# Performance work log

Measured on AMD Instinct MI355X. Metric: run time of the kernel, lower is better.

The kernel has to match this reference:

```python
import jax, jax.numpy as jnp
import numpy as np

N_NODES = 100000
N_EDGES = 1600000
IN_DIM = 64
HIDDEN_DIM = 64


def setup_inputs() -> dict:
    key = jax.random.key(0)
    ks = jax.random.split(key, 8)
    x = jax.random.normal(ks[0], (N_NODES, IN_DIM), dtype=jnp.float32)
    edge_index = jax.random.randint(ks[1], (2, N_EDGES), 0, N_NODES, dtype=jnp.int32)
    s = 1.0 / np.sqrt(IN_DIM)
    sh = 1.0 / np.sqrt(HIDDEN_DIM)
    # SAGEConv params: lin_l (applied to mean-aggregated neighbors, with bias),
    # lin_r (applied to root/self features, no bias) -- PyG defaults.
    w1l = jax.random.uniform(ks[2], (IN_DIM, HIDDEN_DIM), jnp.float32, -s, s)
    b1l = jax.random.uniform(ks[3], (HIDDEN_DIM,), jnp.float32, -s, s)
    w1r = jax.random.uniform(ks[4], (IN_DIM, HIDDEN_DIM), jnp.float32, -s, s)
    w2l = jax.random.uniform(ks[5], (HIDDEN_DIM, HIDDEN_DIM), jnp.float32, -sh, sh)
    b2l = jax.random.uniform(ks[6], (HIDDEN_DIM,), jnp.float32, -sh, sh)
    w2r = jax.random.uniform(ks[7], (HIDDEN_DIM, HIDDEN_DIM), jnp.float32, -sh, sh)
    return {"x": x, "edge_index": edge_index, "w1l": w1l, "b1l": b1l,
            "w1r": w1r, "w2l": w2l, "b2l": b2l, "w2r": w2r}


def reference(x, edge_index, w1l, b1l, w1r, w2l, b2l, w2r):
    n = x.shape[0]
    src, dst = edge_index[0], edge_index[1]
    # in-degree (number of incoming messages per target node), clamped to 1
    deg = jax.ops.segment_sum(jnp.ones(src.shape, x.dtype), dst, num_segments=n)
    inv_deg = 1.0 / jnp.maximum(deg, 1.0)  # [N]

    def sage_conv(h, wl, bl, wr):
        # mean aggregation of neighbor messages: scatter-add then normalize
        agg = jax.ops.segment_sum(h[src], dst, num_segments=n) * inv_deg[:, None]
        return agg @ wl + bl + h @ wr

    h = jax.nn.relu(sage_conv(x, w1l, b1l, w1r))  # conv1 + relu
    return sage_conv(h, w2l, b2l, w2r)            # conv2 (no activation)
```

## Files before the change

kernel.cpp:

```cpp
#include <hip/hip_runtime.h>
#include <hip/hip_fp16.h>


#define DIM 64
#define BN 64
#define MAXBUCK 2048
#define CHUNK 8192
#define GCAP 2048
#define WT_STRIDE 72

using f16x8 = __attribute__((ext_vector_type(8))) _Float16;
using f32x4 = __attribute__((ext_vector_type(4))) float;

__device__ inline void addh8(float* acc, float4 raw) {
    const __half2* hp = (const __half2*)&raw;
#pragma unroll
    for (int k = 0; k < 4; ++k) {
        float2 f = __half22float2(hp[k]);
        acc[2 * k]     += f.x;
        acc[2 * k + 1] += f.y;
    }
}

__global__ __launch_bounds__(256) void prehist_kernel(const int* __restrict__ dst,
                                                      int* __restrict__ ghist,
                                                      int nE, int nbuck) {
    __shared__ int hist[MAXBUCK];
    const int t = threadIdx.x;
    for (int k = t; k < nbuck; k += 256) hist[k] = 0;
    __syncthreads();
    const int base = blockIdx.x * CHUNK;
    const int end = min(nE, base + CHUNK);
    for (int i = base + t; i < end; i += 256)
        atomicAdd(&hist[dst[i] >> 6], 1);
    __syncthreads();
    for (int k = t; k < nbuck; k += 256)
        if (hist[k]) atomicAdd(&ghist[k], hist[k]);
}

__global__ __launch_bounds__(1024) void scan_kernel(const int* __restrict__ ghist,
                                                    int* __restrict__ boff,
                                                    int* __restrict__ gcur, int nbuck) {
    __shared__ int sa[2048], sb[2048];
    const int t = threadIdx.x;
    int v0 = (t < nbuck) ? ghist[t] : 0;
    int v1 = (t + 1024 < nbuck) ? ghist[t + 1024] : 0;
    sa[t] = v0; sa[t + 1024] = v1;
    __syncthreads();
    int* in = sa; int* out = sb;
    for (int d = 1; d < 2048; d <<= 1) {
        out[t] = in[t] + ((t >= d) ? in[t - d] : 0);
        int i2 = t + 1024;
        out[i2] = in[i2] + ((i2 >= d) ? in[i2 - d] : 0);
        __syncthreads();
        int* tmp = in; in = out; out = tmp;
    }
    if (t < nbuck) { int e = in[t] - v0; boff[t] = e; gcur[t] = e; }
    if (t + 1024 < nbuck) { int e = in[t + 1024] - v1; boff[t + 1024] = e; gcur[t + 1024] = e; }
    if (t == 0) boff[nbuck] = in[2047];
}

__device__ inline void load_bfrag(const __half* __restrict__ H, long long nn, int lq,
                                  f16x8& b0, f16x8& b1) {
    b0 = *(const f16x8*)&H[nn * 64 + lq * 8];
    b1 = *(const f16x8*)&H[nn * 64 + 32 + lq * 8];
}
__device__ inline void load_bfrag(const float* __restrict__ H, long long nn, int lq,
                                  f16x8& b0, f16x8& b1) {
    const float* p = &H[nn * 64 + lq * 8];
    float4 u0 = *(const float4*)p;
    float4 u1 = *(const float4*)(p + 4);
    float4 u2 = *(const float4*)(p + 32);
    float4 u3 = *(const float4*)(p + 36);
    b0[0] = (_Float16)u0.x; b0[1] = (_Float16)u0.y; b0[2] = (_Float16)u0.z; b0[3] = (_Float16)u0.w;
    b0[4] = (_Float16)u1.x; b0[5] = (_Float16)u1.y; b0[6] = (_Float16)u1.z; b0[7] = (_Float16)u1.w;
    b1[0] = (_Float16)u2.x; b1[1] = (_Float16)u2.y; b1[2] = (_Float16)u2.z; b1[3] = (_Float16)u2.w;
    b1[4] = (_Float16)u3.x; b1[5] = (_Float16)u3.y; b1[6] = (_Float16)u3.z; b1[7] = (_Float16)u3.w;
}

template <typename InT>
__device__ void gemm_body(int bid, __half* wt,
                          const InT* __restrict__ H,
                          const float* __restrict__ Wl, const float* __restrict__ Wr,
                          const float* __restrict__ bias,
                          __half* __restrict__ A, __half* __restrict__ Dbuf, int n) {
    const int t = threadIdx.x;
    for (int i = t; i < 4096; i += 256) {
        int k = i >> 6, m = i & 63;
        wt[(size_t)m * WT_STRIDE + k] = __float2half(Wl[i]);
        wt[(size_t)(64 + m) * WT_STRIDE + k] = __float2half(Wr[i]);
    }
    __syncthreads();
    const int lane = t & 63, wave = t >> 6;
    const int ln = lane & 15, lq = lane >> 4;
    f16x8 af[2][4][2];
#pragma unroll
    for (int mat = 0; mat < 2; ++mat)
#pragma unroll
        for (int mt = 0; mt < 4; ++mt)
#pragma unroll
            for (int ki = 0; ki < 2; ++ki)
                af[mat][mt][ki] = *(const f16x8*)&wt[(size_t)(mat * 64 + mt * 16 + ln) * WT_STRIDE
                                                     + ki * 32 + lq * 8];
    float4 bf[4];
#pragma unroll
    for (int mt = 0; mt < 4; ++mt)
        bf[mt] = *(const float4*)&bias[mt * 16 + lq * 4];

    const int base = bid * 256;
    for (int it = 0; it < 4; ++it) {
        const int node = base + it * 64 + wave * 16 + ln;
        const long long nn = (node < n) ? node : (n - 1);
        f16x8 b0, b1;
        load_bfrag(H, nn, lq, b0, b1);
        f32x4 acc[2][4];
#pragma unroll
        for (int mat = 0; mat < 2; ++mat)
#pragma unroll
            for (int mt = 0; mt < 4; ++mt) {
                f32x4 z = {0.f, 0.f, 0.f, 0.f};
                z = __builtin_amdgcn_mfma_f32_16x16x32_f16(af[mat][mt][0], b0, z, 0, 0, 0);
                z = __builtin_amdgcn_mfma_f32_16x16x32_f16(af[mat][mt][1], b1, z, 0, 0, 0);
                acc[mat][mt] = z;
            }
        if (node < n) {
#pragma unroll
            for (int mt = 0; mt < 4; ++mt) {
                union { __half2 h[2]; float2 f; } u;
                u.h[0] = __floats2half2_rn(acc[0][mt][0], acc[0][mt][1]);
                u.h[1] = __floats2half2_rn(acc[0][mt][2], acc[0][mt][3]);
                *(float2*)&A[(size_t)node * 64 + mt * 16 + lq * 4] = u.f;
                union { __half2 h[2]; float2 f; } v;
                v.h[0] = __floats2half2_rn(acc[1][mt][0] + bf[mt].x, acc[1][mt][1] + bf[mt].y);
                v.h[1] = __floats2half2_rn(acc[1][mt][2] + bf[mt].z, acc[1][mt][3] + bf[mt].w);
                *(float2*)&Dbuf[(size_t)node * 64 + mt * 16 + lq * 4] = v.f;
            }
        }
    }
}

__global__ __launch_bounds__(256) void part_gemm_kernel(const int* __restrict__ src,
                                                        const int* __restrict__ dst,
                                                        int* __restrict__ gcur,
                                                        unsigned* __restrict__ P,
                                                        int nE, int nbuck, int pb,
                                                        const float* __restrict__ H,
                                                        const float* __restrict__ Wl,
                                                        const float* __restrict__ Wr,
                                                        const float* __restrict__ bias,
                                                        __half* __restrict__ A,
                                                        __half* __restrict__ Dbuf, int n) {
    __shared__ __align__(16) unsigned short smem_u[2 * 64 * WT_STRIDE];
    if ((int)blockIdx.x < pb) {
        int* hist = (int*)smem_u;
        const int t = threadIdx.x;
        for (int k = t; k < nbuck; k += 256) hist[k] = 0;
        __syncthreads();
        const int base = blockIdx.x * CHUNK;
        const int end = min(nE, base + CHUNK);
        for (int i = base + t; i < end; i += 256)
            atomicAdd(&hist[dst[i] >> 6], 1);
        __syncthreads();
        for (int k = t; k < nbuck; k += 256) {
            int h = hist[k];
            hist[k] = h ? atomicAdd(&gcur[k], h) : 0;
        }
        __syncthreads();
        for (int i = base + t; i < end; i += 256) {
            int d = dst[i];
            int bk = d >> 6;
            int pos = atomicAdd(&hist[bk], 1);
            P[pos] = ((unsigned)src[i] << 6) | (unsigned)(d & 63);
        }
    } else {
        gemm_body(blockIdx.x - pb, (__half*)smem_u, H, Wl, Wr, bias, A, Dbuf, n);
    }
}

__global__ __launch_bounds__(256) void gemm_kernel(const __half* __restrict__ H,
                                                   const float* __restrict__ Wl,
                                                   const float* __restrict__ Wr,
                                                   const float* __restrict__ bias,
                                                   __half* __restrict__ A,
                                                   __half* __restrict__ Dbuf, int n) {
    __shared__ __align__(16) unsigned short smem_u[2 * 64 * WT_STRIDE];
    gemm_body(blockIdx.x, (__half*)smem_u, H, Wl, Wr, bias, A, Dbuf, n);
}

template <bool RELU, typename OutT>
__global__ __launch_bounds__(256) void gather_sort_combine(const __half* __restrict__ A,
                                                           const __half* __restrict__ Dbuf,
                                                           const int* __restrict__ boff,
                                                           const unsigned* __restrict__ P,
                                                           int* __restrict__ spill,
                                                           OutT* __restrict__ out, int n) {
    __shared__ int hist[BN];
    __shared__ int rstart[BN];
    __shared__ int cur[BN];
    __shared__ int lsrc[GCAP];
    const int t = threadIdx.x;
    const int b = blockIdx.x;
    if (t < BN) hist[t] = 0;
    __syncthreads();
    const int start = boff[b], end = boff[b + 1];
    const int m = end - start;
    for (int i = start + t; i < end; i += 256)
        atomicAdd(&hist[P[i] & 63], 1);
    __syncthreads();
    if (t < 64) {
        int v = hist[t];
        int s = v;
#pragma unroll
        for (int d = 1; d < 64; d <<= 1) {
            int u = __shfl_up(s, d);
            if (t >= d) s += u;
        }
        rstart[t] = s - v;
        cur[t] = s - v;
    }
    __syncthreads();
    int* list = (m <= GCAP) ? (int*)lsrc : (spill + start);
    for (int i = start + t; i < end; i += 256) {
        unsigned p = P[i];
        int pos = atomicAdd(&cur[p & 63], 1);
        list[pos] = (int)(p >> 6);
    }
    __syncthreads();
    const int dg = t & 7;
    const size_t doff = (size_t)dg * 8;
    for (int pass = 0; pass < 2; ++pass) {
        const int r = pass * 32 + (t >> 3);
        const int node = b * BN + r;
        if (node >= n) continue;
        const int c = hist[r];
        const int* sp = list + rstart[r];
        float acc[8] = {0.f, 0.f, 0.f, 0.f, 0.f, 0.f, 0.f, 0.f};
        int j = 0;
        for (; j + 4 <= c; j += 4) {
            int e0 = sp[j + 0], e1 = sp[j + 1], e2 = sp[j + 2], e3 = sp[j + 3];
            float4 r0 = *(const float4*)&A[(size_t)e0 * 64 + doff];
            float4 r1 = *(const float4*)&A[(size_t)e1 * 64 + doff];
            float4 r2 = *(const float4*)&A[(size_t)e2 * 64 + doff];
            float4 r3 = *(const float4*)&A[(size_t)e3 * 64 + doff];
            addh8(acc, r0); addh8(acc, r1); addh8(acc, r2); addh8(acc, r3);
        }
        for (; j < c; ++j) {
            float4 rr = *(const float4*)&A[(size_t)sp[j] * 64 + doff];
            addh8(acc, rr);
        }
        const float inv = 1.0f / fmaxf((float)c, 1.0f);
        float d8[8] = {0, 0, 0, 0, 0, 0, 0, 0};
        addh8(d8, *(const float4*)&Dbuf[(size_t)node * 64 + doff]);
        float o[8];
#pragma unroll
        for (int k = 0; k < 8; ++k) {
            float v = fmaf(acc[k], inv, d8[k]);
            o[k] = RELU ? fmaxf(v, 0.f) : v;
        }
        if constexpr (sizeof(OutT) == 2) {
            union { __half2 h[4]; float4 f; } u;
#pragma unroll
            for (int k = 0; k < 4; ++k)
                u.h[k] = __floats2half2_rn(o[2 * k], o[2 * k + 1]);
            *(float4*)&out[(size_t)node * 64 + doff] = u.f;
        } else {
            *(float4*)&out[(size_t)node * 64 + doff]     = make_float4(o[0], o[1], o[2], o[3]);
            *(float4*)&out[(size_t)node * 64 + doff + 4] = make_float4(o[4], o[5], o[6], o[7]);
        }
    }
}

extern "C" void kernel_launch(void* const* d_in, const int* in_sizes, int n_in,
                              void* d_out, int out_size, void* d_ws, size_t ws_size,
                              hipStream_t stream) {
    const float* x   = (const float*)d_in[0];
    const int*   ei  = (const int*)d_in[1];
    const float* w1l = (const float*)d_in[2];
    const float* b1l = (const float*)d_in[3];
    const float* w1r = (const float*)d_in[4];
    const float* w2l = (const float*)d_in[5];
    const float* b2l = (const float*)d_in[6];
    const float* w2r = (const float*)d_in[7];
    float* out = (float*)d_out;

    const int N = in_sizes[0] / DIM;
    const int E = in_sizes[1] / 2;
    const int* src = ei;
    const int* dst = ei + E;
    const int nbuck = (N + BN - 1) / BN;
    const int pb = (E + CHUNK - 1) / CHUNK;
    const int gb = (N + 255) / 256;

    int* ghist = (int*)d_ws;
    int* boff = ghist + nbuck;
    int* gcur = boff + nbuck + 1;
    unsigned* P = (unsigned*)(gcur + nbuck);
    int* spill = (int*)(P + E);
    uintptr_t ap = (uintptr_t)(spill + E);
    ap = (ap + 15) & ~(uintptr_t)15;
    __half* A  = (__half*)ap;
    __half* D  = A + (size_t)N * DIM;
    __half* h1 = D + (size_t)N * DIM;

    hipMemsetAsync(ghist, 0, nbuck * sizeof(int), stream);
    prehist_kernel<<<pb, 256, 0, stream>>>(dst, ghist, E, nbuck);
    scan_kernel<<<1, 1024, 0, stream>>>(ghist, boff, gcur, nbuck);
    part_gemm_kernel<<<pb + gb, 256, 0, stream>>>(src, dst, gcur, P, E, nbuck, pb,
                                                  x, w1l, w1r, b1l, A, D, N);

    gather_sort_combine<true, __half><<<nbuck, 256, 0, stream>>>(A, D, boff, P, spill, h1, N);

    gemm_kernel<<<gb, 256, 0, stream>>>(h1, w2l, w2r, b2l, A, D, N);
    gather_sort_combine<false, float><<<nbuck, 256, 0, stream>>>(A, D, boff, P, spill, out, N);
}
```

Baseline: 271.2 us.

## Store per-block bucket histograms and scan them to deterministic partition bases

The histogram kernel now writes each chunk's per-bucket counts to a block-by-bucket matrix. A new kernel uses wave-level prefix sums to turn that matrix into per-block write bases. The partition pass therefore no longer recomputes the histogram or takes global atomic reservations; it loads its bases and scatters directly. CHUNK is halved, which doubles the number of partition blocks and adds an extra kernel launch plus a matrix write and read (roughly pb*nbuck ints).

```diff
diff --git a/kernel.cpp b/kernel.cpp
--- a/kernel.cpp
+++ b/kernel.cpp
@@ -5,7 +5,7 @@
 #define DIM 64
 #define BN 64
 #define MAXBUCK 2048
-#define CHUNK 8192
+#define CHUNK 4096
 #define GCAP 2048
 #define WT_STRIDE 72
 
@@ -22,9 +22,10 @@
     }
 }
 
-__global__ __launch_bounds__(256) void prehist_kernel(const int* __restrict__ dst,
-                                                      int* __restrict__ ghist,
-                                                      int nE, int nbuck) {
+__global__ __launch_bounds__(256) void hist_kernel(const int* __restrict__ dst,
+                                                   int* __restrict__ Hmat,
+                                                   int* __restrict__ ghist,
+                                                   int nE, int nbuck) {
     __shared__ int hist[MAXBUCK];
     const int t = threadIdx.x;
     for (int k = t; k < nbuck; k += 256) hist[k] = 0;
@@ -34,13 +35,16 @@
     for (int i = base + t; i < end; i += 256)
         atomicAdd(&hist[dst[i] >> 6], 1);
     __syncthreads();
-    for (int k = t; k < nbuck; k += 256)
-        if (hist[k]) atomicAdd(&ghist[k], hist[k]);
+    int* row = Hmat + (size_t)blockIdx.x * nbuck;
+    for (int k = t; k < nbuck; k += 256) {
+        int h = hist[k];
+        row[k] = h;
+        if (h) atomicAdd(&ghist[k], h);
+    }
 }
 
 __global__ __launch_bounds__(1024) void scan_kernel(const int* __restrict__ ghist,
-                                                    int* __restrict__ boff,
-                                                    int* __restrict__ gcur, int nbuck) {
+                                                    int* __restrict__ boff, int nbuck) {
     __shared__ int sa[2048], sb[2048];
     const int t = threadIdx.x;
     int v0 = (t < nbuck) ? ghist[t] : 0;
@@ -55,9 +59,30 @@
         __syncthreads();
         int* tmp = in; in = out; out = tmp;
     }
-    if (t < nbuck) { int e = in[t] - v0; boff[t] = e; gcur[t] = e; }
-    if (t + 1024 < nbuck) { int e = in[t + 1024] - v1; boff[t + 1024] = e; gcur[t + 1024] = e; }
+    if (t < nbuck) boff[t] = in[t] - v0;
+    if (t + 1024 < nbuck) boff[t + 1024] = in[t + 1024] - v1;
     if (t == 0) boff[nbuck] = in[2047];
+}
+
+__global__ __launch_bounds__(256) void bases_kernel(int* __restrict__ Hmat,
+                                                    const int* __restrict__ boff,
+                                                    int nbuck, int nblk) {
+    const int k = blockIdx.x * 4 + (threadIdx.x >> 6);
+    if (k >= nbuck) return;
+    const int lane = threadIdx.x & 63;
+    int run = boff[k];
+    for (int j0 = 0; j0 < nblk; j0 += 64) {
+        int j = j0 + lane;
+        int v = (j < nblk) ? Hmat[(size_t)j * nbuck + k] : 0;
+        int s = v;
+#pragma unroll
+        for (int d = 1; d < 64; d <<= 1) {
+            int u = __shfl_up(s, d);
+            if (lane >= d) s += u;
+        }
+        if (j < nblk) Hmat[(size_t)j * nbuck + k] = run + (s - v);
+        run += __shfl(s, 63);
+    }
 }
 
 __device__ inline void load_bfrag(const __half* __restrict__ H, long long nn, int lq,
@@ -141,7 +166,7 @@
 
 __global__ __launch_bounds__(256) void part_gemm_kernel(const int* __restrict__ src,
                                                         const int* __restrict__ dst,
-                                                        int* __restrict__ gcur,
+                                                        const int* __restrict__ Hmat,
                                                         unsigned* __restrict__ P,
                                                         int nE, int nbuck, int pb,
                                                         const float* __restrict__ H,
@@ -152,24 +177,17 @@
                                                         __half* __restrict__ Dbuf, int n) {
     __shared__ __align__(16) unsigned short smem_u[2 * 64 * WT_STRIDE];
     if ((int)blockIdx.x < pb) {
-        int* hist = (int*)smem_u;
+        int* cur = (int*)smem_u;
         const int t = threadIdx.x;
-        for (int k = t; k < nbuck; k += 256) hist[k] = 0;
+        const int* row = Hmat + (size_t)blockIdx.x * nbuck;
+        for (int k = t; k < nbuck; k += 256) cur[k] = row[k];
         __syncthreads();
         const int base = blockIdx.x * CHUNK;
         const int end = min(nE, base + CHUNK);
-        for (int i = base + t; i < end; i += 256)
-            atomicAdd(&hist[dst[i] >> 6], 1);
-        __syncthreads();
-        for (int k = t; k < nbuck; k += 256) {
-            int h = hist[k];
-            hist[k] = h ? atomicAdd(&gcur[k], h) : 0;
-        }
-        __syncthreads();
         for (int i = base + t; i < end; i += 256) {
             int d = dst[i];
             int bk = d >> 6;
-            int pos = atomicAdd(&hist[bk], 1);
+            int pos = atomicAdd(&cur[bk], 1);
             P[pos] = ((unsigned)src[i] << 6) | (unsigned)(d & 63);
         }
     } else {
@@ -293,8 +311,8 @@
 
     int* ghist = (int*)d_ws;
     int* boff = ghist + nbuck;
-    int* gcur = boff + nbuck + 1;
-    unsigned* P = (unsigned*)(gcur + nbuck);
+    int* Hmat = boff + nbuck + 1;
+    unsigned* P = (unsigned*)(Hmat + (size_t)pb * nbuck);
     int* spill = (int*)(P + E);
     uintptr_t ap = (uintptr_t)(spill + E);
     ap = (ap + 15) & ~(uintptr_t)15;
@@ -303,9 +321,11 @@
     __half* h1 = D + (size_t)N * DIM;
 
     hipMemsetAsync(ghist, 0, nbuck * sizeof(int), stream);
-    prehist_kernel<<<pb, 256, 0, stream>>>(dst, ghist, E, nbuck);
-    scan_kernel<<<1, 1024, 0, stream>>>(ghist, boff, gcur, nbuck);
-    part_gemm_kernel<<<pb + gb, 256, 0, stream>>>(src, dst, gcur, P, E, nbuck, pb,
+    hist_kernel<<<pb, 256, 0, stream>>>(dst, Hmat, ghist, E, nbuck);
+    scan_kernel<<<1, 1024, 0, stream>>>(ghist, boff, nbuck);
+    bases_kernel<<<(nbuck + 3) / 4, 256, 0, stream>>>(Hmat, boff, nbuck, pb);
+
+    part_gemm_kernel<<<pb + gb, 256, 0, stream>>>(src, dst, Hmat, P, E, nbuck, pb,
                                                   x, w1l, w1r, b1l, A, D, N);
 
     gather_sort_combine<true, __half><<<nbuck, 256, 0, stream>>>(A, D, boff, P, spill, h1, N);
```

Result: no change. 276.4 us (+1.9%).
